# Kernel tuning notes

Measured on AMD Instinct MI355X. Metric: run time of the kernel, lower is better.

## Reference

```python
import jax
import jax.numpy as jnp
from jax import lax
import numpy as np

N, D, V, T = 16384, 256, 32000, 128
U_DECAY = 0.97


def _ln_row(z, eps=1e-6):
    # torch layernorm_row: (z - mean) / (std_unbiased + eps)
    m = z.mean(axis=-1, keepdims=True)
    s = z.std(axis=-1, ddof=1, keepdims=True)  # torch .std is unbiased
    return (z - m) / (s + eps)


def setup_inputs() -> dict:
    key = jax.random.key(0)
    k0, k1, k2, k3, k4 = jax.random.split(key, 5)
    E = jax.random.normal(k0, (D, N), dtype=jnp.float32) / np.sqrt(N).astype(np.float32)
    Dx = jax.random.normal(k1, (N, D), dtype=jnp.float32) / np.sqrt(D).astype(np.float32)
    Dy = jax.random.normal(k2, (N, D), dtype=jnp.float32) / np.sqrt(D).astype(np.float32)
    token_emb = jax.random.normal(k3, (V, D), dtype=jnp.float32) / np.sqrt(D).astype(np.float32)
    tokens = jax.random.randint(k4, (T,), 0, V)
    return {"E": E, "Dx": Dx, "Dy": Dy, "token_emb": token_emb, "tokens": tokens}


def reference(E, Dx, Dy, token_emb, tokens):
    d, n = E.shape

    def step(carry, tok):
        x, rho = carry
        v_prev = token_emb[tok]                    # [d]
        x_t = x + jax.nn.relu(Dx @ v_prev)         # [n], use_relu_lowrank=True
        a_star = rho @ x_t                         # [d]
        y_core = Dy @ _ln_row(a_star)              # [n], ln_before_Dy=True
        y_t = jax.nn.relu(y_core) * jnp.maximum(x_t, 0.0)
        v_star = _ln_row(E @ y_t)                  # [d]
        rho = U_DECAY * (rho + jnp.outer(v_prev, x_t))  # rank-1 write + decay
        return (x_t, rho), (y_t, v_star)

    x0 = jnp.zeros((n,), dtype=E.dtype)
    rho0 = jnp.zeros((d, n), dtype=E.dtype)
    (x_f, rho_f), (ys, vs) = lax.scan(step, (x0, rho0), tokens)
    # final states x, y, v, rho concatenated into one vector
    return jnp.concatenate([x_f, ys[-1], vs[-1], rho_f.ravel()])
```

## Files before the change

### kernel.cpp

```cpp
#include <hip/hip_runtime.h>
#include <cstddef>

namespace {
constexpr int Nn = 16384;
constexpr int Dd = 256;
constexpr int Tt = 128;
constexpr float DECAY = 0.97f;

constexpr size_t WS_M    = 0;
constexpr size_t WS_CUMV = WS_M + (size_t)Nn * Tt;
constexpr size_t WS_H    = WS_CUMV + (size_t)Tt * Dd;
constexpr size_t WS_LNA  = WS_H + Tt;
constexpr size_t WS_U    = WS_LNA + Dd;
}

__global__ __launch_bounds__(256) void k_p1(const float* __restrict__ Dx,
                                            const float* __restrict__ temb,
                                            const int* __restrict__ toks,
                                            float* __restrict__ Mg,
                                            float* __restrict__ cumV,
                                            float* __restrict__ h,
                                            float* __restrict__ xf) {
  __shared__ int s_toks[Tt];
  __shared__ __align__(16) float As[32 * 32];
  __shared__ __align__(16) float Bs[32 * 128];
  __shared__ float xjl[32];

  const int tid = threadIdx.x;
  const int b = blockIdx.x;
  if (tid < Tt) s_toks[tid] = toks[tid];
  __syncthreads();

  if (b < Tt) {
    const int s = b;
    float run = 0.f, w = DECAY;
    for (int t = Tt - 1; t >= s; --t) {
      run += w * temb[(size_t)s_toks[t] * Dd + tid];
      w *= DECAY;
    }
    cumV[s * Dd + tid] = run;
    return;
  }

  const int j0 = (b - Tt) * 32;
  const int tx = tid & 15, ty = tid >> 4;
  const float4* Dx4 = (const float4*)Dx;
  const float4* T4 = (const float4*)temb;
  float acc[2][8] = {};

  const int arow = tid >> 3, ak4 = tid & 7;
  auto loadA = [&](int ch) {
    return Dx4[(size_t)(j0 + arow) * 64 + ch * 8 + ak4];
  };
  auto loadB = [&](int ch, int i) {
    int idx = tid + i * 256, t = idx >> 3, k4 = idx & 7;
    return T4[(size_t)s_toks[t] * 64 + ch * 8 + k4];
  };
  float4 pa = loadA(0);
  float4 pb[4] = {loadB(0, 0), loadB(0, 1), loadB(0, 2), loadB(0, 3)};

  for (int ch = 0; ch < 8; ++ch) {
    __syncthreads();
    {
      const int asw = arow ^ (8 * (ak4 & 3));
      As[(ak4 * 4 + 0) * 32 + asw] = pa.x;
      As[(ak4 * 4 + 1) * 32 + asw] = pa.y;
      As[(ak4 * 4 + 2) * 32 + asw] = pa.z;
      As[(ak4 * 4 + 3) * 32 + asw] = pa.w;
    }
#pragma unroll
    for (int i = 0; i < 4; ++i) {
      int idx = tid + i * 256, t = idx >> 3, k4 = idx & 7;
      const int bsw = t ^ (8 * k4);
      Bs[(k4 * 4 + 0) * 128 + bsw] = pb[i].x;
      Bs[(k4 * 4 + 1) * 128 + bsw] = pb[i].y;
      Bs[(k4 * 4 + 2) * 128 + bsw] = pb[i].z;
      Bs[(k4 * 4 + 3) * 128 + bsw] = pb[i].w;
    }
    __syncthreads();
    if (ch < 7) {
      pa = loadA(ch + 1);
      pb[0] = loadB(ch + 1, 0); pb[1] = loadB(ch + 1, 1);
      pb[2] = loadB(ch + 1, 2); pb[3] = loadB(ch + 1, 3);
    }
#pragma unroll
    for (int kk = 0; kk < 32; ++kk) {
      const int sA = 8 * ((kk >> 2) & 3);
      const int sB = 8 * (kk >> 2);
      float2 a = *(const float2*)&As[kk * 32 + ((ty * 2) ^ sA)];
      float4 b0 = *(const float4*)&Bs[kk * 128 + ((tx * 8) ^ sB)];
      float4 b1 = *(const float4*)&Bs[kk * 128 + ((tx * 8) ^ sB) + 4];
      float avv[2] = {a.x, a.y};
      float bvv[8] = {b0.x, b0.y, b0.z, b0.w, b1.x, b1.y, b1.z, b1.w};
#pragma unroll
      for (int r = 0; r < 2; ++r)
#pragma unroll
        for (int c = 0; c < 8; ++c) acc[r][c] += avv[r] * bvv[c];
    }
  }

  float rs[2];
#pragma unroll
  for (int r = 0; r < 2; ++r) {
    float s = 0.f;
#pragma unroll
    for (int c = 0; c < 8; ++c) {
      acc[r][c] = fmaxf(acc[r][c], 0.f);
      s += acc[r][c];
    }
    rs[r] = s;
    int j = j0 + ty * 2 + r;
    float4 o0 = {acc[r][0], acc[r][1], acc[r][2], acc[r][3]};
    float4 o1 = {acc[r][4], acc[r][5], acc[r][6], acc[r][7]};
    *(float4*)&Mg[(size_t)j * Tt + tx * 8] = o0;
    *(float4*)&Mg[(size_t)j * Tt + tx * 8 + 4] = o1;
  }
  __syncthreads();
  float* redx = As;
#pragma unroll
  for (int r = 0; r < 2; ++r) redx[(ty * 2 + r) * 17 + tx] = rs[r];
  __syncthreads();
  if (tid < 32) {
    float s = 0.f;
#pragma unroll
    for (int x = 0; x < 16; ++x) s += redx[tid * 17 + x];
    xjl[tid] = s;
    xf[j0 + tid] = s;
  }
  __syncthreads();
  float* hred = Bs;
#pragma unroll
  for (int c = 0; c < 8; ++c) {
    float p = acc[0][c] * xjl[ty * 2] + acc[1][c] * xjl[ty * 2 + 1];
    hred[(tx * 8 + c) * 17 + ty] = p;
  }
  __syncthreads();
  if (tid < Tt) {
    float s = 0.f;
#pragma unroll
    for (int i = 0; i < 16; ++i) s += hred[tid * 17 + i];
    atomicAdd(&h[tid], s);
  }
}

__global__ __launch_bounds__(256) void k_astar(const float* __restrict__ h,
                                               const float* __restrict__ temb,
                                               const int* __restrict__ toks,
                                               float* __restrict__ lna) {
  __shared__ float g[Tt];
  __shared__ float red[Dd];
  __shared__ int s_toks[Tt];
  const int d = threadIdx.x;
  if (d < Tt) {
    s_toks[d] = toks[d];
    g[d] = h[d];
  }
  __syncthreads();
  for (int off = 1; off < Tt; off <<= 1) {
    float v = 0.f;
    bool act = (d < Tt) && (d >= off);
    if (act) v = g[d - off];
    __syncthreads();
    if (act) g[d] += v;
    __syncthreads();
  }
  float a = 0.f, w = DECAY;
  for (int t = Tt - 2; t >= 0; --t) {
    a += w * g[t] * temb[(size_t)s_toks[t] * Dd + d];
    w *= DECAY;
  }
  red[d] = a;
  __syncthreads();
  for (int off = 128; off > 0; off >>= 1) {
    if (d < off) red[d] += red[d + off];
    __syncthreads();
  }
  float m = red[0] * (1.f / 256.f);
  __syncthreads();
  float c0 = a - m;
  red[d] = c0 * c0;
  __syncthreads();
  for (int off = 128; off > 0; off >>= 1) {
    if (d < off) red[d] += red[d + off];
    __syncthreads();
  }
  float sd = sqrtf(red[0] * (1.f / 255.f));
  lna[d] = c0 / (sd + 1e-6f);
}

__global__ void k_y(const float* __restrict__ Dy, const float* __restrict__ lna,
                    const float* __restrict__ x, float* __restrict__ yout) {
  const int tid = threadIdx.x;
  const int wave = tid >> 6, lane = tid & 63;
  const int j = blockIdx.x * 4 + wave;
  const float4* Dy4 = (const float4*)Dy;
  const float4* l4 = (const float4*)lna;
  float4 a = Dy4[(size_t)j * 64 + lane];
  float4 bq = l4[lane];
  float acc = a.x * bq.x + a.y * bq.y + a.z * bq.z + a.w * bq.w;
#pragma unroll
  for (int off = 32; off > 0; off >>= 1) acc += __shfl_down(acc, off);
  if (lane == 0) yout[j] = fmaxf(acc, 0.f) * fmaxf(x[j], 0.f);
}

__global__ void k_u(const float* __restrict__ E, const float* __restrict__ y,
                    float* __restrict__ u) {
  __shared__ float red[256];
  const int d = blockIdx.x, tid = threadIdx.x;
  const float4* E4 = (const float4*)E;
  const float4* y4 = (const float4*)y;
  float acc = 0.f;
  for (int i = 0; i < 16; ++i) {
    int idx = tid + i * 256;
    float4 e = E4[(size_t)d * 4096 + idx];
    float4 yv = y4[idx];
    acc += e.x * yv.x + e.y * yv.y + e.z * yv.z + e.w * yv.w;
  }
  red[tid] = acc;
  __syncthreads();
  for (int off = 128; off > 0; off >>= 1) {
    if (tid < off) red[tid] += red[tid + off];
    __syncthreads();
  }
  if (tid == 0) u[d] = red[0];
}

__global__ __launch_bounds__(256) void k_rho(const float* __restrict__ cumV,
                                             const float* __restrict__ Mg,
                                             const float* __restrict__ u,
                                             float* __restrict__ rho,
                                             float* __restrict__ vs) {
  __shared__ __align__(16) float As[32 * 64];
  __shared__ __align__(16) float Bs[32 * 128];
  __shared__ float red[Dd];
  const int tid = threadIdx.x;
  const int b = blockIdx.x;

  if (b == 0) {
    float a = u[tid];
    red[tid] = a;
    __syncthreads();
    for (int off = 128; off > 0; off >>= 1) {
      if (tid < off) red[tid] += red[tid + off];
      __syncthreads();
    }
    float m = red[0] * (1.f / 256.f);
    __syncthreads();
    float c0 = a - m;
    red[tid] = c0 * c0;
    __syncthreads();
    for (int off = 128; off > 0; off >>= 1) {
      if (tid < off) red[tid] += red[tid + off];
      __syncthreads();
    }
    float sd = sqrtf(red[0] * (1.f / 255.f));
    vs[tid] = c0 / (sd + 1e-6f);
  }

  const int d0 = (b & 3) * 64;
  const int j0 = (b >> 2) * 128;
  const int tx = tid & 15, ty = tid >> 4;
  float acc[4][8] = {};
  const float4* C4 = (const float4*)cumV;
  const float4* M4 = (const float4*)Mg;
  const int ak = tid >> 4, ad4 = tid & 15;
  auto loadRA = [&](int ch, int i) {
    return C4[(size_t)(ch * 32 + ak + i * 16) * 64 + (d0 >> 2) + ad4];
  };
  auto loadRB = [&](int ch, int i) {
    int idx = tid + i * 256, j = idx >> 3, k4 = idx & 7;
    return M4[(size_t)(j0 + j) * 32 + ch * 8 + k4];
  };
  float4 qa[2] = {loadRA(0, 0), loadRA(0, 1)};
  float4 qb[4] = {loadRB(0, 0), loadRB(0, 1), loadRB(0, 2), loadRB(0, 3)};

  for (int ch = 0; ch < 4; ++ch) {
    __syncthreads();
#pragma unroll
    for (int i = 0; i < 2; ++i)
      *(float4*)&As[(ak + i * 16) * 64 + ad4 * 4] = qa[i];
#pragma unroll
    for (int i = 0; i < 4; ++i) {
      int idx = tid + i * 256, j = idx >> 3, k4 = idx & 7;
      const int bsw = j ^ (8 * k4);
      Bs[(k4 * 4 + 0) * 128 + bsw] = qb[i].x;
      Bs[(k4 * 4 + 1) * 128 + bsw] = qb[i].y;
      Bs[(k4 * 4 + 2) * 128 + bsw] = qb[i].z;
      Bs[(k4 * 4 + 3) * 128 + bsw] = qb[i].w;
    }
    __syncthreads();
    if (ch < 3) {
      qa[0] = loadRA(ch + 1, 0); qa[1] = loadRA(ch + 1, 1);
      qb[0] = loadRB(ch + 1, 0); qb[1] = loadRB(ch + 1, 1);
      qb[2] = loadRB(ch + 1, 2); qb[3] = loadRB(ch + 1, 3);
    }
#pragma unroll
    for (int kk = 0; kk < 32; ++kk) {
      const int sB = 8 * (kk >> 2);
      float4 a = *(const float4*)&As[kk * 64 + ty * 4];
      float4 b0 = *(const float4*)&Bs[kk * 128 + ((tx * 8) ^ sB)];
      float4 b1 = *(const float4*)&Bs[kk * 128 + ((tx * 8) ^ sB) + 4];
      float avv[4] = {a.x, a.y, a.z, a.w};
      float bvv[8] = {b0.x, b0.y, b0.z, b0.w, b1.x, b1.y, b1.z, b1.w};
#pragma unroll
      for (int r = 0; r < 4; ++r)
#pragma unroll
        for (int c = 0; c < 8; ++c) acc[r][c] += avv[r] * bvv[c];
    }
  }
#pragma unroll
  for (int r = 0; r < 4; ++r) {
    int d = d0 + ty * 4 + r;
    float4 o0 = {acc[r][0], acc[r][1], acc[r][2], acc[r][3]};
    float4 o1 = {acc[r][4], acc[r][5], acc[r][6], acc[r][7]};
    *(float4*)&rho[(size_t)d * Nn + j0 + tx * 8] = o0;
    *(float4*)&rho[(size_t)d * Nn + j0 + tx * 8 + 4] = o1;
  }
}

extern "C" void kernel_launch(void* const* d_in, const int* in_sizes, int n_in,
                              void* d_out, int out_size, void* d_ws, size_t ws_size,
                              hipStream_t stream) {
  const float* E = (const float*)d_in[0];
  const float* Dx = (const float*)d_in[1];
  const float* Dy = (const float*)d_in[2];
  const float* temb = (const float*)d_in[3];
  const int* toks = (const int*)d_in[4];

  float* ws = (float*)d_ws;
  float* out = (float*)d_out;
  float* Mg   = ws + WS_M;
  float* cumV = ws + WS_CUMV;
  float* h    = ws + WS_H;
  float* lna  = ws + WS_LNA;
  float* u    = ws + WS_U;

  float* xf  = out;
  float* yv  = out + Nn;
  float* vs  = out + 2 * Nn;
  float* rho = out + 2 * Nn + Dd;

  hipMemsetAsync(h, 0, (Tt + 2 * Dd) * sizeof(float), stream);

  k_p1<<<Tt + Nn / 32, 256, 0, stream>>>(Dx, temb, toks, Mg, cumV, h, xf);
  k_astar<<<1, 256, 0, stream>>>(h, temb, toks, lna);
  k_y<<<Nn / 4, 256, 0, stream>>>(Dy, lna, xf, yv);
  k_u<<<Dd, 256, 0, stream>>>(E, yv, u);
  k_rho<<<512, 256, 0, stream>>>(cumV, Mg, u, rho, vs);
}
```

Before: 178.1 us.

## Fuse rho GEMM into phase-1 kernel with bf16 MFMA and drop Mg buffer

After: 185.0 us. 3.9% more time.

```diff
diff --git a/kernel.cpp b/kernel.cpp
--- a/kernel.cpp
+++ b/kernel.cpp
@@ -7,154 +7,206 @@
 constexpr int Tt = 128;
 constexpr float DECAY = 0.97f;
 
-constexpr size_t WS_M    = 0;
-constexpr size_t WS_CUMV = WS_M + (size_t)Nn * Tt;
-constexpr size_t WS_H    = WS_CUMV + (size_t)Tt * Dd;
-constexpr size_t WS_LNA  = WS_H + Tt;
-constexpr size_t WS_U    = WS_LNA + Dd;
+constexpr size_t WS_CUMVT = 0;
+constexpr size_t WS_VB    = 16384;
+constexpr size_t WS_H     = 49152;
+constexpr size_t WS_LNA   = 49280;
+constexpr size_t WS_U     = 49536;
+}
+
+typedef __attribute__((ext_vector_type(8))) short short8;
+typedef __attribute__((ext_vector_type(4))) short short4v;
+typedef __attribute__((ext_vector_type(4))) float f32x4;
+typedef unsigned short u16;
+
+__device__ __forceinline__ u16 f2bf(float f) {
+  unsigned u = __builtin_bit_cast(unsigned, f);
+  return (u16)((u + 0x7fffu + ((u >> 16) & 1u)) >> 16);
+}
+
+__global__ __launch_bounds__(256) void k0(const float* __restrict__ temb,
+                                          const int* __restrict__ toks,
+                                          u16* __restrict__ cumVT,
+                                          float* __restrict__ Vb) {
+  __shared__ int st[Tt];
+  const int s = blockIdx.x, d = threadIdx.x;
+  if (d < Tt) st[d] = toks[d];
+  __syncthreads();
+  float run = 0.f, w = DECAY, v = 0.f;
+  for (int t = Tt - 1; t >= s; --t) {
+    v = temb[(size_t)st[t] * Dd + d];
+    run += w * v;
+    w *= DECAY;
+  }
+  Vb[s * Dd + d] = v;
+  cumVT[d * Tt + s] = f2bf(run);
 }
 
 __global__ __launch_bounds__(256) void k_p1(const float* __restrict__ Dx,
-                                            const float* __restrict__ temb,
-                                            const int* __restrict__ toks,
-                                            float* __restrict__ Mg,
-                                            float* __restrict__ cumV,
+                                            const float* __restrict__ Vb,
+                                            const u16* __restrict__ cumVT,
                                             float* __restrict__ h,
-                                            float* __restrict__ xf) {
-  __shared__ int s_toks[Tt];
-  __shared__ __align__(16) float As[32 * 32];
-  __shared__ __align__(16) float Bs[32 * 128];
+                                            float* __restrict__ xf,
+                                            float* __restrict__ rho) {
+  __shared__ __align__(16) u16 Asl[32 * 40];
+  __shared__ __align__(16) u16 Bsl[128 * 40];
+  __shared__ __align__(16) u16 Mld[32 * 136];
+  __shared__ __align__(16) u16 CVl[64 * 136];
+  __shared__ float xpart[4][16];
+  __shared__ float hpart[4][64];
   __shared__ float xjl[32];
 
   const int tid = threadIdx.x;
-  const int b = blockIdx.x;
-  if (tid < Tt) s_toks[tid] = toks[tid];
-  __syncthreads();
-
-  if (b < Tt) {
-    const int s = b;
-    float run = 0.f, w = DECAY;
-    for (int t = Tt - 1; t >= s; --t) {
-      run += w * temb[(size_t)s_toks[t] * Dd + tid];
-      w *= DECAY;
-    }
-    cumV[s * Dd + tid] = run;
-    return;
-  }
-
-  const int j0 = (b - Tt) * 32;
-  const int tx = tid & 15, ty = tid >> 4;
+  const int j0 = blockIdx.x * 32;
+  const int w = tid >> 6, l = tid & 63;
+  const int jt = w & 1, thf = w >> 1;
+  const int lr = l & 15, lg = l >> 4;
+
   const float4* Dx4 = (const float4*)Dx;
-  const float4* T4 = (const float4*)temb;
-  float acc[2][8] = {};
-
-  const int arow = tid >> 3, ak4 = tid & 7;
-  auto loadA = [&](int ch) {
-    return Dx4[(size_t)(j0 + arow) * 64 + ch * 8 + ak4];
-  };
-  auto loadB = [&](int ch, int i) {
-    int idx = tid + i * 256, t = idx >> 3, k4 = idx & 7;
-    return T4[(size_t)s_toks[t] * 64 + ch * 8 + k4];
-  };
-  float4 pa = loadA(0);
-  float4 pb[4] = {loadB(0, 0), loadB(0, 1), loadB(0, 2), loadB(0, 3)};
+  const float4* Vb4 = (const float4*)Vb;
+
+  const int ar = tid >> 3, akq = tid & 7;
+  const int btr = tid >> 1, bh = tid & 1;
+
+  f32x4 zero = {0.f, 0.f, 0.f, 0.f};
+  f32x4 acc[4] = {zero, zero, zero, zero};
+
+  float4 pa = Dx4[(size_t)(j0 + ar) * 64 + akq];
+  float4 pb0 = Vb4[(size_t)btr * 64 + bh * 4 + 0];
+  float4 pb1 = Vb4[(size_t)btr * 64 + bh * 4 + 1];
+  float4 pb2 = Vb4[(size_t)btr * 64 + bh * 4 + 2];
+  float4 pb3 = Vb4[(size_t)btr * 64 + bh * 4 + 3];
 
   for (int ch = 0; ch < 8; ++ch) {
     __syncthreads();
     {
-      const int asw = arow ^ (8 * (ak4 & 3));
-      As[(ak4 * 4 + 0) * 32 + asw] = pa.x;
-      As[(ak4 * 4 + 1) * 32 + asw] = pa.y;
-      As[(ak4 * 4 + 2) * 32 + asw] = pa.z;
-      As[(ak4 * 4 + 3) * 32 + asw] = pa.w;
-    }
-#pragma unroll
-    for (int i = 0; i < 4; ++i) {
-      int idx = tid + i * 256, t = idx >> 3, k4 = idx & 7;
-      const int bsw = t ^ (8 * k4);
-      Bs[(k4 * 4 + 0) * 128 + bsw] = pb[i].x;
-      Bs[(k4 * 4 + 1) * 128 + bsw] = pb[i].y;
-      Bs[(k4 * 4 + 2) * 128 + bsw] = pb[i].z;
-      Bs[(k4 * 4 + 3) * 128 + bsw] = pb[i].w;
+      short4v a4;
+      a4[0] = (short)f2bf(pa.x); a4[1] = (short)f2bf(pa.y);
+      a4[2] = (short)f2bf(pa.z); a4[3] = (short)f2bf(pa.w);
+      *(short4v*)&Asl[ar * 40 + akq * 4] = a4;
+    }
+    {
+      short8 b0, b1;
+      b0[0] = (short)f2bf(pb0.x); b0[1] = (short)f2bf(pb0.y);
+      b0[2] = (short)f2bf(pb0.z); b0[3] = (short)f2bf(pb0.w);
+      b0[4] = (short)f2bf(pb1.x); b0[5] = (short)f2bf(pb1.y);
+      b0[6] = (short)f2bf(pb1.z); b0[7] = (short)f2bf(pb1.w);
+      b1[0] = (short)f2bf(pb2.x); b1[1] = (short)f2bf(pb2.y);
+      b1[2] = (short)f2bf(pb2.z); b1[3] = (short)f2bf(pb2.w);
+      b1[4] = (short)f2bf(pb3.x); b1[5] = (short)f2bf(pb3.y);
+      b1[6] = (short)f2bf(pb3.z); b1[7] = (short)f2bf(pb3.w);
+      *(short8*)&Bsl[btr * 40 + bh * 16] = b0;
+      *(short8*)&Bsl[btr * 40 + bh * 16 + 8] = b1;
     }
     __syncthreads();
     if (ch < 7) {
-      pa = loadA(ch + 1);
-      pb[0] = loadB(ch + 1, 0); pb[1] = loadB(ch + 1, 1);
-      pb[2] = loadB(ch + 1, 2); pb[3] = loadB(ch + 1, 3);
-    }
-#pragma unroll
-    for (int kk = 0; kk < 32; ++kk) {
-      const int sA = 8 * ((kk >> 2) & 3);
-      const int sB = 8 * (kk >> 2);
-      float2 a = *(const float2*)&As[kk * 32 + ((ty * 2) ^ sA)];
-      float4 b0 = *(const float4*)&Bs[kk * 128 + ((tx * 8) ^ sB)];
-      float4 b1 = *(const float4*)&Bs[kk * 128 + ((tx * 8) ^ sB) + 4];
-      float avv[2] = {a.x, a.y};
-      float bvv[8] = {b0.x, b0.y, b0.z, b0.w, b1.x, b1.y, b1.z, b1.w};
-#pragma unroll
-      for (int r = 0; r < 2; ++r)
-#pragma unroll
-        for (int c = 0; c < 8; ++c) acc[r][c] += avv[r] * bvv[c];
-    }
-  }
-
-  float rs[2];
-#pragma unroll
-  for (int r = 0; r < 2; ++r) {
-    float s = 0.f;
-#pragma unroll
-    for (int c = 0; c < 8; ++c) {
-      acc[r][c] = fmaxf(acc[r][c], 0.f);
-      s += acc[r][c];
-    }
-    rs[r] = s;
-    int j = j0 + ty * 2 + r;
-    float4 o0 = {acc[r][0], acc[r][1], acc[r][2], acc[r][3]};
-    float4 o1 = {acc[r][4], acc[r][5], acc[r][6], acc[r][7]};
-    *(float4*)&Mg[(size_t)j * Tt + tx * 8] = o0;
-    *(float4*)&Mg[(size_t)j * Tt + tx * 8 + 4] = o1;
-  }
-  __syncthreads();
-  float* redx = As;
-#pragma unroll
-  for (int r = 0; r < 2; ++r) redx[(ty * 2 + r) * 17 + tx] = rs[r];
+      pa = Dx4[(size_t)(j0 + ar) * 64 + (ch + 1) * 8 + akq];
+      pb0 = Vb4[(size_t)btr * 64 + (ch + 1) * 8 + bh * 4 + 0];
+      pb1 = Vb4[(size_t)btr * 64 + (ch + 1) * 8 + bh * 4 + 1];
+      pb2 = Vb4[(size_t)btr * 64 + (ch + 1) * 8 + bh * 4 + 2];
+      pb3 = Vb4[(size_t)btr * 64 + (ch + 1) * 8 + bh * 4 + 3];
+    }
+    short8 av = *(const short8*)&Asl[(jt * 16 + lr) * 40 + lg * 8];
+#pragma unroll
+    for (int tt = 0; tt < 4; ++tt) {
+      short8 bv = *(const short8*)&Bsl[((thf * 4 + tt) * 16 + lr) * 40 + lg * 8];
+      acc[tt] = __builtin_amdgcn_mfma_f32_16x16x32_bf16(av, bv, acc[tt], 0, 0, 0);
+    }
+  }
+
+#pragma unroll
+  for (int tt = 0; tt < 4; ++tt)
+#pragma unroll
+    for (int q = 0; q < 4; ++q) {
+      float vv = fmaxf(acc[tt][q], 0.f);
+      acc[tt][q] = vv;
+      Mld[(jt * 16 + lg * 4 + q) * 136 + thf * 64 + tt * 16 + lr] = f2bf(vv);
+    }
+
+  float p0 = acc[0][0] + acc[1][0] + acc[2][0] + acc[3][0];
+  float p1 = acc[0][1] + acc[1][1] + acc[2][1] + acc[3][1];
+  float p2 = acc[0][2] + acc[1][2] + acc[2][2] + acc[3][2];
+  float p3 = acc[0][3] + acc[1][3] + acc[2][3] + acc[3][3];
+#pragma unroll
+  for (int m = 1; m <= 8; m <<= 1) {
+    p0 += __shfl_xor(p0, m); p1 += __shfl_xor(p1, m);
+    p2 += __shfl_xor(p2, m); p3 += __shfl_xor(p3, m);
+  }
+  float pv = p0;
+  if (lr == 1) pv = p1; else if (lr == 2) pv = p2; else if (lr == 3) pv = p3;
+  if (lr < 4) xpart[w][lg * 4 + lr] = pv;
   __syncthreads();
   if (tid < 32) {
-    float s = 0.f;
-#pragma unroll
-    for (int x = 0; x < 16; ++x) s += redx[tid * 17 + x];
+    float s = xpart[tid >> 4][tid & 15] + xpart[(tid >> 4) + 2][tid & 15];
     xjl[tid] = s;
     xf[j0 + tid] = s;
   }
   __syncthreads();
-  float* hred = Bs;
-#pragma unroll
-  for (int c = 0; c < 8; ++c) {
-    float p = acc[0][c] * xjl[ty * 2] + acc[1][c] * xjl[ty * 2 + 1];
-    hred[(tx * 8 + c) * 17 + ty] = p;
+
+  float xq0 = xjl[jt * 16 + lg * 4 + 0];
+  float xq1 = xjl[jt * 16 + lg * 4 + 1];
+  float xq2 = xjl[jt * 16 + lg * 4 + 2];
+  float xq3 = xjl[jt * 16 + lg * 4 + 3];
+  float ph0 = acc[0][0]*xq0 + acc[0][1]*xq1 + acc[0][2]*xq2 + acc[0][3]*xq3;
+  float ph1 = acc[1][0]*xq0 + acc[1][1]*xq1 + acc[1][2]*xq2 + acc[1][3]*xq3;
+  float ph2 = acc[2][0]*xq0 + acc[2][1]*xq1 + acc[2][2]*xq2 + acc[2][3]*xq3;
+  float ph3 = acc[3][0]*xq0 + acc[3][1]*xq1 + acc[3][2]*xq2 + acc[3][3]*xq3;
+#pragma unroll
+  for (int m = 16; m <= 32; m <<= 1) {
+    ph0 += __shfl_xor(ph0, m); ph1 += __shfl_xor(ph1, m);
+    ph2 += __shfl_xor(ph2, m); ph3 += __shfl_xor(ph3, m);
+  }
+  if (l < 16) {
+    hpart[w][l] = ph0; hpart[w][16 + l] = ph1;
+    hpart[w][32 + l] = ph2; hpart[w][48 + l] = ph3;
   }
   __syncthreads();
   if (tid < Tt) {
-    float s = 0.f;
-#pragma unroll
-    for (int i = 0; i < 16; ++i) s += hred[tid * 17 + i];
-    atomicAdd(&h[tid], s);
+    int half = tid >> 6;
+    atomicAdd(&h[tid], hpart[half * 2][tid & 63] + hpart[half * 2 + 1][tid & 63]);
+  }
+
+  const float4* CV4 = (const float4*)cumVT;
+  float4 q0 = CV4[tid], q1 = CV4[tid + 256], q2 = CV4[tid + 512],
+         q3 = CV4[tid + 768];
+  for (int dc = 0; dc < 4; ++dc) {
+    __syncthreads();
+    *(float4*)&CVl[(tid >> 4) * 136 + (tid & 15) * 8] = q0;
+    *(float4*)&CVl[((tid + 256) >> 4) * 136 + (tid & 15) * 8] = q1;
+    *(float4*)&CVl[((tid + 512) >> 4) * 136 + (tid & 15) * 8] = q2;
+    *(float4*)&CVl[((tid + 768) >> 4) * 136 + (tid & 15) * 8] = q3;
+    __syncthreads();
+    if (dc < 3) {
+      q0 = CV4[(dc + 1) * 1024 + tid];
+      q1 = CV4[(dc + 1) * 1024 + tid + 256];
+      q2 = CV4[(dc + 1) * 1024 + tid + 512];
+      q3 = CV4[(dc + 1) * 1024 + tid + 768];
+    }
+    f32x4 r0 = zero, r1 = zero;
+#pragma unroll
+    for (int ks = 0; ks < 4; ++ks) {
+      short8 a = *(const short8*)&CVl[(w * 16 + lr) * 136 + ks * 32 + lg * 8];
+      short8 b0 = *(const short8*)&Mld[lr * 136 + ks * 32 + lg * 8];
+      short8 b1 = *(const short8*)&Mld[(16 + lr) * 136 + ks * 32 + lg * 8];
+      r0 = __builtin_amdgcn_mfma_f32_16x16x32_bf16(a, b0, r0, 0, 0, 0);
+      r1 = __builtin_amdgcn_mfma_f32_16x16x32_bf16(a, b1, r1, 0, 0, 0);
+    }
+#pragma unroll
+    for (int q = 0; q < 4; ++q) {
+      size_t drow = (size_t)(dc * 64 + w * 16 + lg * 4 + q) * Nn;
+      rho[drow + j0 + lr] = r0[q];
+      rho[drow + j0 + 16 + lr] = r1[q];
+    }
   }
 }
 
 __global__ __launch_bounds__(256) void k_astar(const float* __restrict__ h,
-                                               const float* __restrict__ temb,
-                                               const int* __restrict__ toks,
+                                               const float* __restrict__ Vb,
                                                float* __restrict__ lna) {
   __shared__ float g[Tt];
   __shared__ float red[Dd];
-  __shared__ int s_toks[Tt];
   const int d = threadIdx.x;
-  if (d < Tt) {
-    s_toks[d] = toks[d];
-    g[d] = h[d];
-  }
+  if (d < Tt) g[d] = h[d];
   __syncthreads();
   for (int off = 1; off < Tt; off <<= 1) {
     float v = 0.f;
@@ -164,10 +216,10 @@
     if (act) g[d] += v;
     __syncthreads();
   }
-  float a = 0.f, w = DECAY;
+  float a = 0.f, wv = DECAY;
   for (int t = Tt - 2; t >= 0; --t) {
-    a += w * g[t] * temb[(size_t)s_toks[t] * Dd + d];
-    w *= DECAY;
+    a += wv * g[t] * Vb[t * Dd + d];
+    wv *= DECAY;
   }
   red[d] = a;
   __syncthreads();
@@ -206,12 +258,13 @@
 __global__ void k_u(const float* __restrict__ E, const float* __restrict__ y,
                     float* __restrict__ u) {
   __shared__ float red[256];
-  const int d = blockIdx.x, tid = threadIdx.x;
+  const int d = blockIdx.x >> 1, hf = blockIdx.x & 1, tid = threadIdx.x;
   const float4* E4 = (const float4*)E;
   const float4* y4 = (const float4*)y;
   float acc = 0.f;
-  for (int i = 0; i < 16; ++i) {
-    int idx = tid + i * 256;
+#pragma unroll
+  for (int i = 0; i < 8; ++i) {
+    int idx = hf * 2048 + tid + i * 256;
     float4 e = E4[(size_t)d * 4096 + idx];
     float4 yv = y4[idx];
     acc += e.x * yv.x + e.y * yv.y + e.z * yv.z + e.w * yv.w;
@@ -222,100 +275,30 @@
     if (tid < off) red[tid] += red[tid + off];
     __syncthreads();
   }
-  if (tid == 0) u[d] = red[0];
-}
-
-__global__ __launch_bounds__(256) void k_rho(const float* __restrict__ cumV,
-                                             const float* __restrict__ Mg,
-                                             const float* __restrict__ u,
-                                             float* __restrict__ rho,
-                                             float* __restrict__ vs) {
-  __shared__ __align__(16) float As[32 * 64];
-  __shared__ __align__(16) float Bs[32 * 128];
-  __shared__ float red[Dd];
-  const int tid = threadIdx.x;
-  const int b = blockIdx.x;
-
-  if (b == 0) {
-    float a = u[tid];
-    red[tid] = a;
-    __syncthreads();
-    for (int off = 128; off > 0; off >>= 1) {
-      if (tid < off) red[tid] += red[tid + off];
-      __syncthreads();
-    }
-    float m = red[0] * (1.f / 256.f);
-    __syncthreads();
-    float c0 = a - m;
-    red[tid] = c0 * c0;
-    __syncthreads();
-    for (int off = 128; off > 0; off >>= 1) {
-      if (tid < off) red[tid] += red[tid + off];
-      __syncthreads();
-    }
-    float sd = sqrtf(red[0] * (1.f / 255.f));
-    vs[tid] = c0 / (sd + 1e-6f);
-  }
-
-  const int d0 = (b & 3) * 64;
-  const int j0 = (b >> 2) * 128;
-  const int tx = tid & 15, ty = tid >> 4;
-  float acc[4][8] = {};
-  const float4* C4 = (const float4*)cumV;
-  const float4* M4 = (const float4*)Mg;
-  const int ak = tid >> 4, ad4 = tid & 15;
-  auto loadRA = [&](int ch, int i) {
-    return C4[(size_t)(ch * 32 + ak + i * 16) * 64 + (d0 >> 2) + ad4];
-  };
-  auto loadRB = [&](int ch, int i) {
-    int idx = tid + i * 256, j = idx >> 3, k4 = idx & 7;
-    return M4[(size_t)(j0 + j) * 32 + ch * 8 + k4];
-  };
-  float4 qa[2] = {loadRA(0, 0), loadRA(0, 1)};
-  float4 qb[4] = {loadRB(0, 0), loadRB(0, 1), loadRB(0, 2), loadRB(0, 3)};
-
-  for (int ch = 0; ch < 4; ++ch) {
-    __syncthreads();
-#pragma unroll
-    for (int i = 0; i < 2; ++i)
-      *(float4*)&As[(ak + i * 16) * 64 + ad4 * 4] = qa[i];
-#pragma unroll
-    for (int i = 0; i < 4; ++i) {
-      int idx = tid + i * 256, j = idx >> 3, k4 = idx & 7;
-      const int bsw = j ^ (8 * k4);
-      Bs[(k4 * 4 + 0) * 128 + bsw] = qb[i].x;
-      Bs[(k4 * 4 + 1) * 128 + bsw] = qb[i].y;
-      Bs[(k4 * 4 + 2) * 128 + bsw] = qb[i].z;
-      Bs[(k4 * 4 + 3) * 128 + bsw] = qb[i].w;
-    }
-    __syncthreads();
-    if (ch < 3) {
-      qa[0] = loadRA(ch + 1, 0); qa[1] = loadRA(ch + 1, 1);
-      qb[0] = loadRB(ch + 1, 0); qb[1] = loadRB(ch + 1, 1);
-      qb[2] = loadRB(ch + 1, 2); qb[3] = loadRB(ch + 1, 3);
-    }
-#pragma unroll
-    for (int kk = 0; kk < 32; ++kk) {
-      const int sB = 8 * (kk >> 2);
-      float4 a = *(const float4*)&As[kk * 64 + ty * 4];
-      float4 b0 = *(const float4*)&Bs[kk * 128 + ((tx * 8) ^ sB)];
-      float4 b1 = *(const float4*)&Bs[kk * 128 + ((tx * 8) ^ sB) + 4];
-      float avv[4] = {a.x, a.y, a.z, a.w};
-      float bvv[8] = {b0.x, b0.y, b0.z, b0.w, b1.x, b1.y, b1.z, b1.w};
-#pragma unroll
-      for (int r = 0; r < 4; ++r)
-#pragma unroll
-        for (int c = 0; c < 8; ++c) acc[r][c] += avv[r] * bvv[c];
-    }
-  }
-#pragma unroll
-  for (int r = 0; r < 4; ++r) {
-    int d = d0 + ty * 4 + r;
-    float4 o0 = {acc[r][0], acc[r][1], acc[r][2], acc[r][3]};
-    float4 o1 = {acc[r][4], acc[r][5], acc[r][6], acc[r][7]};
-    *(float4*)&rho[(size_t)d * Nn + j0 + tx * 8] = o0;
-    *(float4*)&rho[(size_t)d * Nn + j0 + tx * 8 + 4] = o1;
-  }
+  if (tid == 0) atomicAdd(&u[d], red[0]);
+}
+
+__global__ void k_v(const float* __restrict__ u, float* __restrict__ vout) {
+  __shared__ float red[256];
+  const int d = threadIdx.x;
+  float a = u[d];
+  red[d] = a;
+  __syncthreads();
+  for (int off = 128; off > 0; off >>= 1) {
+    if (d < off) red[d] += red[d + off];
+    __syncthreads();
+  }
+  float m = red[0] * (1.f / 256.f);
+  __syncthreads();
+  float c0 = a - m;
+  red[d] = c0 * c0;
+  __syncthreads();
+  for (int off = 128; off > 0; off >>= 1) {
+    if (d < off) red[d] += red[d + off];
+    __syncthreads();
+  }
+  float sd = sqrtf(red[0] * (1.f / 255.f));
+  vout[d] = c0 / (sd + 1e-6f);
 }
 
 extern "C" void kernel_launch(void* const* d_in, const int* in_sizes, int n_in,
@@ -329,11 +312,11 @@
 
   float* ws = (float*)d_ws;
   float* out = (float*)d_out;
-  float* Mg   = ws + WS_M;
-  float* cumV = ws + WS_CUMV;
-  float* h    = ws + WS_H;
-  float* lna  = ws + WS_LNA;
-  float* u    = ws + WS_U;
+  u16* cumVT = (u16*)(ws + WS_CUMVT);
+  float* Vb  = ws + WS_VB;
+  float* h   = ws + WS_H;
+  float* lna = ws + WS_LNA;
+  float* u   = ws + WS_U;
 
   float* xf  = out;
   float* yv  = out + Nn;
@@ -342,9 +325,10 @@
 
   hipMemsetAsync(h, 0, (Tt + 2 * Dd) * sizeof(float), stream);
 
-  k_p1<<<Tt + Nn / 32, 256, 0, stream>>>(Dx, temb, toks, Mg, cumV, h, xf);
-  k_astar<<<1, 256, 0, stream>>>(h, temb, toks, lna);
+  k0<<<Tt, 256, 0, stream>>>(temb, toks, cumVT, Vb);
+  k_p1<<<Nn / 32, 256, 0, stream>>>(Dx, Vb, cumVT, h, xf, rho);
+  k_astar<<<1, 256, 0, stream>>>(h, Vb, lna);
   k_y<<<Nn / 4, 256, 0, stream>>>(Dy, lna, xf, yv);
-  k_u<<<Dd, 256, 0, stream>>>(E, yv, u);
-  k_rho<<<512, 256, 0, stream>>>(cumV, Mg, u, rho, vs);
-}
+  k_u<<<2 * Dd, 256, 0, stream>>>(E, yv, u);
+  k_v<<<1, 256, 0, stream>>>(u, vs);
+}
```
